# Optimization experiments

Measured on AMD Instinct MI355X. Metric: run time of the kernel, lower is better.

## Reference

```python
import jax, jax.numpy as jnp
import numpy as np

KERNEL_SIZE = 7
DILATION = 1
DYNAMIC_SIZE = 3


def setup_inputs() -> dict:
    key = jax.random.key(0)
    # [B, 2*(channels+1), H, W]; channels = 8 filterable + (8+2) param channels
    x = jax.random.normal(key, (2, 18, 1024, 1024), dtype=jnp.float32)
    return {"input": x}


def _bilateral(filterable, params, kernel_size, dilation):
    # filterable: [B, C, H, W]; params: [B, C+2, H, W] (already negated squares)
    B, C, H, W = filterable.shape
    r = kernel_size // 2
    pad = r * dilation
    fp = jnp.pad(filterable, ((0, 0), (0, 0), (pad, pad), (pad, pad)))
    mp = jnp.pad(jnp.ones((B, 1, H, W), filterable.dtype),
                 ((0, 0), (0, 0), (pad, pad), (pad, pad)))  # validity mask
    range_p = params[:, :C]      # per-channel range coefficients (<= 0)
    sx = params[:, C]            # spatial x coefficient (<= 0)
    sy = params[:, C + 1]        # spatial y coefficient (<= 0)
    acc = jnp.zeros_like(filterable)
    wsum = jnp.zeros((B, H, W), filterable.dtype)
    for i in range(kernel_size):        # fixed small window: loop is structural
        for j in range(kernel_size):
            oy, ox = i * dilation, j * dilation
            fn = jax.lax.dynamic_slice(fp, (0, 0, oy, ox), (B, C, H, W))
            m = jax.lax.dynamic_slice(mp, (0, 0, oy, ox), (B, 1, H, W))[:, 0]
            d2 = (fn - filterable) ** 2
            dy2 = float(((i - r) * dilation) ** 2)
            dx2 = float(((j - r) * dilation) ** 2)
            logw = jnp.einsum('bchw,bchw->bhw', range_p, d2) + sx * dx2 + sy * dy2
            w = jnp.exp(logw) * m   # out-of-bounds taps masked to 0
            acc = acc + w[:, None] * fn
            wsum = wsum + w
    # center tap has weight exp(0)=1, so wsum >= 1 (no div-by-zero)
    return acc / wsum[:, None]


def reference(input):
    C_in = input.shape[1]
    channels = C_in // 2 - 1
    filterable = input[:, :channels]
    params = input[:, channels:]
    params = -(params * params)
    filtered = _bilateral(filterable, params, KERNEL_SIZE, DILATION)
    return filtered[:, :DYNAMIC_SIZE]
```

## Files before the change

### kernel.cpp

```cpp
#include <hip/hip_runtime.h>

namespace {

constexpr int H = 1024;
constexpr int W = 1024;
constexpr int PLANE = H * W;
constexpr int CIN = 18;
constexpr int C = 8;
constexpr int TX = 16;
constexpr int TY = 16;
constexpr int TILE_H = 32;
constexpr int SW = TX + 6;
constexpr int SH = TILE_H + 6;
constexpr int NPOS = SW * SH;
constexpr float LOG2E = 1.44269504088896340736f;

typedef _Float16 half2_t __attribute__((ext_vector_type(2)));
typedef _Float16 half8_t __attribute__((ext_vector_type(8)));

__device__ __forceinline__ float dot2acc(half2_t a, half2_t b, float c) {
#if defined(__has_builtin)
#if __has_builtin(__builtin_amdgcn_fdot2)
    return __builtin_amdgcn_fdot2(a, b, c, false);
#else
    return fmaf((float)a[0], (float)b[0], fmaf((float)a[1], (float)b[1], c));
#endif
#else
    return fmaf((float)a[0], (float)b[0], fmaf((float)a[1], (float)b[1], c));
#endif
}

__device__ __forceinline__ float fast_exp2(float x) {
#if defined(__has_builtin)
#if __has_builtin(__builtin_amdgcn_exp2f)
    return __builtin_amdgcn_exp2f(x);
#else
    return exp2f(x);
#endif
#else
    return exp2f(x);
#endif
}

template<bool INTERIOR>
__device__ __forceinline__ void run_tile(const float* __restrict__ inb,
                                         float* __restrict__ outb,
                                         half8_t* __restrict__ tile,
                                         float* __restrict__ msk,
                                         int gy0, int gx0)
{
    const int tx = threadIdx.x, ty = threadIdx.y;
    const int tid = ty * TX + tx;

    const int o0 = gy0 + 2 * ty;
    const int gx = gx0 + tx;
    const int pofs0 = o0 * W + gx;

    half2_t rp01_0, rp23_0, rp45_0, rp67_0;
    half2_t rp01_1, rp23_1, rp45_1, rp67_1;
    float sxf0, syf0, sxf1, syf1;
    {
        const float* pp = inb + (size_t)C * PLANE + pofs0;
#define PAIR(DST0, DST1, CA, CB) do {                                     \
        float a0_ = pp[(size_t)(CA) * PLANE];                             \
        float b0_ = pp[(size_t)(CB) * PLANE];                             \
        float a1_ = pp[(size_t)(CA) * PLANE + W];                         \
        float b1_ = pp[(size_t)(CB) * PLANE + W];                         \
        DST0 = half2_t{(_Float16)(-(a0_ * a0_) * LOG2E),                  \
                       (_Float16)(-(b0_ * b0_) * LOG2E)};                 \
        DST1 = half2_t{(_Float16)(-(a1_ * a1_) * LOG2E),                  \
                       (_Float16)(-(b1_ * b1_) * LOG2E)};                 \
    } while (0)
        PAIR(rp01_0, rp01_1, 0, 1);
        PAIR(rp23_0, rp23_1, 2, 3);
        PAIR(rp45_0, rp45_1, 4, 5);
        PAIR(rp67_0, rp67_1, 6, 7);
#undef PAIR
        float px0 = pp[(size_t)8 * PLANE];
        float py0 = pp[(size_t)9 * PLANE];
        float px1 = pp[(size_t)8 * PLANE + W];
        float py1 = pp[(size_t)9 * PLANE + W];
        sxf0 = -(px0 * px0) * LOG2E;  syf0 = -(py0 * py0) * LOG2E;
        sxf1 = -(px1 * px1) * LOG2E;  syf1 = -(py1 * py1) * LOG2E;
    }

#pragma unroll 1
    for (int idx = tid; idx < NPOS; idx += TX * TY) {
        int y = idx / SW;
        int x = idx - y * SW;
        int sy_ = gy0 + y - 3;
        int sx_ = gx0 + x - 3;
        half8_t hv;
        if (INTERIOR || ((unsigned)sy_ < (unsigned)H && (unsigned)sx_ < (unsigned)W)) {
            const float* p = inb + sy_ * W + sx_;
#pragma unroll
            for (int c = 0; c < C; ++c) hv[c] = (_Float16)p[(size_t)c * PLANE];
            if (!INTERIOR) msk[idx] = 1.0f;
        } else {
#pragma unroll
            for (int c = 0; c < C; ++c) hv[c] = (_Float16)0.0f;
            msk[idx] = 0.0f;
        }
        tile[idx] = hv;
    }
    __syncthreads();

    const half8_t* lp = tile + (2 * ty) * SW + tx;
    const half8_t fc0 = lp[3 * SW + 3];
    const half8_t fc1 = lp[4 * SW + 3];

    float a00 = 0.f, a01 = 0.f, a02 = 0.f, ws0 = 0.f;
    float a10 = 0.f, a11 = 0.f, a12 = 0.f, ws1 = 0.f;

#define PIX(Q, RP01, RP23, RP45, RP67, SXF, RS, MUL, WS, A0, A1, A2, J) do { \
        half8_t d_ = (Q) - (MUL);                                        \
        half8_t dd_ = d_ * d_;                                           \
        float lw_ = fmaf((float)(((J) - 3) * ((J) - 3)), (SXF), (RS));   \
        lw_ = dot2acc(__builtin_shufflevector(dd_, dd_, 0, 1), RP01, lw_); \
        lw_ = dot2acc(__builtin_shufflevector(dd_, dd_, 2, 3), RP23, lw_); \
        lw_ = dot2acc(__builtin_shufflevector(dd_, dd_, 4, 5), RP45, lw_); \
        lw_ = dot2acc(__builtin_shufflevector(dd_, dd_, 6, 7), RP67, lw_); \
        float w_ = fast_exp2(lw_);                                       \
        if (!INTERIOR) w_ *= mrow_[(J)];                                 \
        WS += w_;                                                        \
        A0 = fmaf(w_, (float)(Q)[0], A0);                                \
        A1 = fmaf(w_, (float)(Q)[1], A1);                                \
        A2 = fmaf(w_, (float)(Q)[2], A2);                                \
    } while (0)

#pragma unroll 1
    for (int i = 0; i < 8; ++i) {
        const half8_t* lq_ = lp + i * SW;
        half8_t q0_ = lq_[0], q1_ = lq_[1], q2_ = lq_[2], q3_ = lq_[3],
                q4_ = lq_[4], q5_ = lq_[5], q6_ = lq_[6];
        const float* mrow_ = msk + (2 * ty + i) * SW + tx;
        (void)mrow_;
        if (i != 7) {
            const float rs0_ = syf0 * (float)((i - 3) * (i - 3));
            PIX(q0_, rp01_0, rp23_0, rp45_0, rp67_0, sxf0, rs0_, fc0, ws0, a00, a01, a02, 0);
            PIX(q1_, rp01_0, rp23_0, rp45_0, rp67_0, sxf0, rs0_, fc0, ws0, a00, a01, a02, 1);
            PIX(q2_, rp01_0, rp23_0, rp45_0, rp67_0, sxf0, rs0_, fc0, ws0, a00, a01, a02, 2);
            PIX(q3_, rp01_0, rp23_0, rp45_0, rp67_0, sxf0, rs0_, fc0, ws0, a00, a01, a02, 3);
            PIX(q4_, rp01_0, rp23_0, rp45_0, rp67_0, sxf0, rs0_, fc0, ws0, a00, a01, a02, 4);
            PIX(q5_, rp01_0, rp23_0, rp45_0, rp67_0, sxf0, rs0_, fc0, ws0, a00, a01, a02, 5);
            PIX(q6_, rp01_0, rp23_0, rp45_0, rp67_0, sxf0, rs0_, fc0, ws0, a00, a01, a02, 6);
        }
        if (i != 0) {
            const float rs1_ = syf1 * (float)((i - 4) * (i - 4));
            PIX(q0_, rp01_1, rp23_1, rp45_1, rp67_1, sxf1, rs1_, fc1, ws1, a10, a11, a12, 0);
            PIX(q1_, rp01_1, rp23_1, rp45_1, rp67_1, sxf1, rs1_, fc1, ws1, a10, a11, a12, 1);
            PIX(q2_, rp01_1, rp23_1, rp45_1, rp67_1, sxf1, rs1_, fc1, ws1, a10, a11, a12, 2);
            PIX(q3_, rp01_1, rp23_1, rp45_1, rp67_1, sxf1, rs1_, fc1, ws1, a10, a11, a12, 3);
            PIX(q4_, rp01_1, rp23_1, rp45_1, rp67_1, sxf1, rs1_, fc1, ws1, a10, a11, a12, 4);
            PIX(q5_, rp01_1, rp23_1, rp45_1, rp67_1, sxf1, rs1_, fc1, ws1, a10, a11, a12, 5);
            PIX(q6_, rp01_1, rp23_1, rp45_1, rp67_1, sxf1, rs1_, fc1, ws1, a10, a11, a12, 6);
        }
    }
#undef PIX

    const float inv0 = 1.0f / ws0;
    const float inv1 = 1.0f / ws1;
    outb[pofs0]                 = a00 * inv0;
    outb[PLANE + pofs0]         = a01 * inv0;
    outb[2 * PLANE + pofs0]     = a02 * inv0;
    outb[pofs0 + W]             = a10 * inv1;
    outb[PLANE + pofs0 + W]     = a11 * inv1;
    outb[2 * PLANE + pofs0 + W] = a12 * inv1;
}

__global__ __launch_bounds__(TX * TY, 2) void bilateral_kernel(const float* __restrict__ in,
                                                               float* __restrict__ out)
{
    __shared__ __align__(16) half8_t tile[NPOS];
    __shared__ float msk[NPOS];
    const int b = blockIdx.z;
    const int gx0 = blockIdx.x * TX;
    const int gy0 = blockIdx.y * TILE_H;
    const float* inb = in + (size_t)b * CIN * PLANE;
    float* outb = out + (size_t)b * 3 * PLANE;

    const bool interior = (gx0 >= 3) && (gx0 + TX + 3 <= W) &&
                          (gy0 >= 3) && (gy0 + TILE_H + 3 <= H);
    if (interior)
        run_tile<true>(inb, outb, tile, msk, gy0, gx0);
    else
        run_tile<false>(inb, outb, tile, msk, gy0, gx0);
}

}

extern "C" void kernel_launch(void* const* d_in, const int* in_sizes, int n_in,
                              void* d_out, int out_size, void* d_ws, size_t ws_size,
                              hipStream_t stream)
{
    const float* in = (const float*)d_in[0];
    float* out = (float*)d_out;
    dim3 grid(W / TX, H / TILE_H, 2);
    dim3 block(TX, TY);
    hipLaunchKernelGGL(bilateral_kernel, grid, block, 0, stream, in, out);
}
```

Before: 258.4 us.

## Vectorize halo tile loads, pad LDS pitch, and remap workgroups for XCD locality

Interior tiles now load the halo with float4 global loads. The tile is widened to 24 columns aligned on 4, and one thread per 4-pixel chunk packs 8 channels to fp16, replacing the scalar per-pixel gather loop. The LDS row pitch is padded to 25 to reduce bank conflicts on the stencil reads. The grid is flattened to 1D with a blockIdx permutation so that consecutive tiles land on the same XCD and share L2. Costs are more idle threads during the load phase (228 of 256 active) and slightly wider halo reads.

```diff
diff --git a/kernel.cpp b/kernel.cpp
--- a/kernel.cpp
+++ b/kernel.cpp
@@ -10,13 +10,19 @@
 constexpr int TX = 16;
 constexpr int TY = 16;
 constexpr int TILE_H = 32;
-constexpr int SW = TX + 6;
+constexpr int SWD = 24;
+constexpr int PITCH = 25;
 constexpr int SH = TILE_H + 6;
-constexpr int NPOS = SW * SH;
+constexpr int NREC = SWD * SH;
+constexpr int NCHUNK = 6 * SH;
+constexpr int GX = W / TX;
+constexpr int GY = H / TILE_H;
+constexpr int NWG = GX * GY * 2;
 constexpr float LOG2E = 1.44269504088896340736f;
 
 typedef _Float16 half2_t __attribute__((ext_vector_type(2)));
 typedef _Float16 half8_t __attribute__((ext_vector_type(8)));
+typedef float float4_t __attribute__((ext_vector_type(4)));
 
 __device__ __forceinline__ float dot2acc(half2_t a, half2_t b, float c) {
 #if defined(__has_builtin)
@@ -84,30 +90,56 @@
         sxf1 = -(px1 * px1) * LOG2E;  syf1 = -(py1 * py1) * LOG2E;
     }
 
+    if (INTERIOR) {
+        if (tid < NCHUNK) {
+            int y = tid / 6;
+            int xc = tid - y * 6;
+            const float* p = inb + (size_t)(gy0 - 3 + y) * W + (gx0 - 4 + xc * 4);
+            float4_t v0 = *reinterpret_cast<const float4_t*>(p);
+            float4_t v1 = *reinterpret_cast<const float4_t*>(p + (size_t)1 * PLANE);
+            float4_t v2 = *reinterpret_cast<const float4_t*>(p + (size_t)2 * PLANE);
+            float4_t v3 = *reinterpret_cast<const float4_t*>(p + (size_t)3 * PLANE);
+            float4_t v4 = *reinterpret_cast<const float4_t*>(p + (size_t)4 * PLANE);
+            float4_t v5 = *reinterpret_cast<const float4_t*>(p + (size_t)5 * PLANE);
+            float4_t v6 = *reinterpret_cast<const float4_t*>(p + (size_t)6 * PLANE);
+            float4_t v7 = *reinterpret_cast<const float4_t*>(p + (size_t)7 * PLANE);
+            const int tb = y * PITCH + xc * 4;
+#define PACK(K) do { half8_t h_;                                          \
+            h_[0] = (_Float16)v0[K]; h_[1] = (_Float16)v1[K];             \
+            h_[2] = (_Float16)v2[K]; h_[3] = (_Float16)v3[K];             \
+            h_[4] = (_Float16)v4[K]; h_[5] = (_Float16)v5[K];             \
+            h_[6] = (_Float16)v6[K]; h_[7] = (_Float16)v7[K];             \
+            tile[tb + (K)] = h_; } while (0)
+            PACK(0); PACK(1); PACK(2); PACK(3);
+#undef PACK
+        }
+    } else {
 #pragma unroll 1
-    for (int idx = tid; idx < NPOS; idx += TX * TY) {
-        int y = idx / SW;
-        int x = idx - y * SW;
-        int sy_ = gy0 + y - 3;
-        int sx_ = gx0 + x - 3;
-        half8_t hv;
-        if (INTERIOR || ((unsigned)sy_ < (unsigned)H && (unsigned)sx_ < (unsigned)W)) {
-            const float* p = inb + sy_ * W + sx_;
+        for (int idx = tid; idx < NREC; idx += TX * TY) {
+            int y = idx / SWD;
+            int x = idx - y * SWD;
+            int sy_ = gy0 + y - 3;
+            int sx_ = gx0 + x - 4;
+            half8_t hv;
+            const int sofs = y * PITCH + x;
+            if ((unsigned)sy_ < (unsigned)H && (unsigned)sx_ < (unsigned)W) {
+                const float* p = inb + sy_ * W + sx_;
 #pragma unroll
-            for (int c = 0; c < C; ++c) hv[c] = (_Float16)p[(size_t)c * PLANE];
-            if (!INTERIOR) msk[idx] = 1.0f;
-        } else {
+                for (int c = 0; c < C; ++c) hv[c] = (_Float16)p[(size_t)c * PLANE];
+                msk[sofs] = 1.0f;
+            } else {
 #pragma unroll
-            for (int c = 0; c < C; ++c) hv[c] = (_Float16)0.0f;
-            msk[idx] = 0.0f;
-        }
-        tile[idx] = hv;
+                for (int c = 0; c < C; ++c) hv[c] = (_Float16)0.0f;
+                msk[sofs] = 0.0f;
+            }
+            tile[sofs] = hv;
+        }
     }
     __syncthreads();
 
-    const half8_t* lp = tile + (2 * ty) * SW + tx;
-    const half8_t fc0 = lp[3 * SW + 3];
-    const half8_t fc1 = lp[4 * SW + 3];
+    const half8_t* lp = tile + (2 * ty) * PITCH + (tx + 1);
+    const half8_t fc0 = lp[3 * PITCH + 3];
+    const half8_t fc1 = lp[4 * PITCH + 3];
 
     float a00 = 0.f, a01 = 0.f, a02 = 0.f, ws0 = 0.f;
     float a10 = 0.f, a11 = 0.f, a12 = 0.f, ws1 = 0.f;
@@ -130,10 +162,10 @@
 
 #pragma unroll 1
     for (int i = 0; i < 8; ++i) {
-        const half8_t* lq_ = lp + i * SW;
+        const half8_t* lq_ = lp + i * PITCH;
         half8_t q0_ = lq_[0], q1_ = lq_[1], q2_ = lq_[2], q3_ = lq_[3],
                 q4_ = lq_[4], q5_ = lq_[5], q6_ = lq_[6];
-        const float* mrow_ = msk + (2 * ty + i) * SW + tx;
+        const float* mrow_ = msk + (2 * ty + i) * PITCH + (tx + 1);
         (void)mrow_;
         if (i != 7) {
             const float rs0_ = syf0 * (float)((i - 3) * (i - 3));
@@ -171,15 +203,21 @@
 __global__ __launch_bounds__(TX * TY, 2) void bilateral_kernel(const float* __restrict__ in,
                                                                float* __restrict__ out)
 {
-    __shared__ __align__(16) half8_t tile[NPOS];
-    __shared__ float msk[NPOS];
-    const int b = blockIdx.z;
-    const int gx0 = blockIdx.x * TX;
-    const int gy0 = blockIdx.y * TILE_H;
-    const float* inb = in + (size_t)b * CIN * PLANE;
-    float* outb = out + (size_t)b * 3 * PLANE;
-
-    const bool interior = (gx0 >= 3) && (gx0 + TX + 3 <= W) &&
+    __shared__ __align__(16) half8_t tile[PITCH * SH];
+    __shared__ float msk[PITCH * SH];
+
+    const int bid = blockIdx.x;
+    const int fin = (bid & 7) * (NWG / 8) + (bid >> 3);
+    const int bx = fin & (GX - 1);
+    const int by = (fin >> 6) & (GY - 1);
+    const int bz = fin >> 11;
+
+    const int gx0 = bx * TX;
+    const int gy0 = by * TILE_H;
+    const float* inb = in + (size_t)bz * CIN * PLANE;
+    float* outb = out + (size_t)bz * 3 * PLANE;
+
+    const bool interior = (gx0 >= 4) && (gx0 + TX + 4 <= W) &&
                           (gy0 >= 3) && (gy0 + TILE_H + 3 <= H);
     if (interior)
         run_tile<true>(inb, outb, tile, msk, gy0, gx0);
@@ -195,7 +233,7 @@
 {
     const float* in = (const float*)d_in[0];
     float* out = (float*)d_out;
-    dim3 grid(W / TX, H / TILE_H, 2);
+    dim3 grid(NWG, 1, 1);
     dim3 block(TX, TY);
     hipLaunchKernelGGL(bilateral_kernel, grid, block, 0, stream, in, out);
 }
```

New measurement: 254.8 us. About the same (-1.4%).
